# Performance work log

Measured on AMD Instinct MI355X. Metric: run time of the kernel, lower is better.

The kernel has to match this reference:

```python
import jax, jax.numpy as jnp
import numpy as np

EPS = 1e-6
NUM_SPECIAL = 4
NUM_HEADS = 16


def _rms_norm(x, w, eps=EPS):
    # x: [..., d], normalize over last dim
    var = jnp.mean(jnp.square(x), axis=-1, keepdims=True)
    return x * jax.lax.rsqrt(var + eps) * w


def _rotate_half(x):
    d = x.shape[-1] // 2
    return jnp.concatenate([-x[..., d:], x[..., :d]], axis=-1)


def _apply_rotary(q, k, cos, sin):
    # q,k: [B,H,N,hd]; cos,sin: [N,hd] -> broadcast [1,1,N,hd]
    cos = cos[None, None, :, :]
    sin = sin[None, None, :, :]
    q_out = q * cos + _rotate_half(q) * sin
    k_out = k * cos + _rotate_half(k) * sin
    return q_out, k_out


def _make_2d_mask(seq_len, num_special, window):
    # special tokens attend / are attended fully; patches use 2D local box
    patch_len = seq_len - num_special
    gs = int(round(patch_len ** 0.5))
    idx = jnp.arange(seq_len)
    special = idx < num_special
    p = idx - num_special
    row = p // gs
    col = p % gs
    special_case = special[:, None] | special[None, :]
    swa = (jnp.abs(row[:, None] - row[None, :]) <= window) & (
        jnp.abs(col[:, None] - col[None, :]) <= window)
    return special_case | swa  # [N, N] bool


def setup_inputs() -> dict:
    key = jax.random.key(0)
    ks = jax.random.split(key, 7)
    B, N, C = 4, 1028, 1024
    hd = C // NUM_HEADS
    return {
        "hidden_states": jax.random.normal(ks[0], (B, N, C), dtype=jnp.float32),
        "cos": jax.random.uniform(ks[1], (N, hd), dtype=jnp.float32),
        "sin": jax.random.uniform(ks[2], (N, hd), dtype=jnp.float32),
        "qkv_w": jax.random.normal(ks[3], (3 * C, C), dtype=jnp.float32) * (C ** -0.5),
        "out_w": jax.random.normal(ks[4], (C, C), dtype=jnp.float32) * (C ** -0.5),
        "norm_q_w": jnp.ones((hd,), dtype=jnp.float32),
        "norm_k_w": jnp.ones((hd,), dtype=jnp.float32),
        "sliding_window": 2,
    }


def reference(hidden_states, cos, sin, qkv_w, out_w, norm_q_w, norm_k_w, sliding_window):
    B, N, C = hidden_states.shape
    H = NUM_HEADS
    hd = C // H

    # fused QKV projection (nn.Linear: x @ W^T)
    qkv = jnp.einsum('bnc,dc->bnd', hidden_states, qkv_w)
    qkv = qkv.reshape(B, N, 3, H, hd).transpose(2, 0, 3, 1, 4)  # [3,B,H,N,hd]
    q, k, v = qkv[0], qkv[1], qkv[2]

    # per-head-dim RMSNorm on q and k
    q = _rms_norm(q, norm_q_w)
    k = _rms_norm(k, norm_k_w)

    # RoPE
    q, k = _apply_rotary(q, k, cos, sin)

    # 2D sliding-window + special-token mask
    mask = _make_2d_mask(N, NUM_SPECIAL, sliding_window)  # [N,N]

    scale = 1.0 / jnp.sqrt(jnp.asarray(hd, dtype=q.dtype))
    scores = jnp.einsum('bhqd,bhkd->bhqk', q, k) * scale
    neg = jnp.asarray(jnp.finfo(scores.dtype).min, dtype=scores.dtype)
    scores = jnp.where(mask[None, None, :, :], scores, neg)
    probs = jax.nn.softmax(scores, axis=-1)
    attn = jnp.einsum('bhqk,bhkd->bhqd', probs, v)  # [B,H,N,hd]

    attn = attn.transpose(0, 2, 1, 3).reshape(B, N, C)
    return jnp.einsum('bnc,dc->bnd', attn, out_w)
```

## Files before the change

kernel.cpp:

```cpp
#include <hip/hip_runtime.h>
#include <hip/hip_bf16.h>
#include <stdint.h>

typedef __bf16 bf16;
typedef __attribute__((ext_vector_type(8))) __bf16 bf16x8;
typedef __attribute__((ext_vector_type(4))) __bf16 bf16x4;
typedef __attribute__((ext_vector_type(4))) float f32x4;

#define NSEQ 1028
#define CDIM 1024
#define NHEADS 16
#define HD 64
#define BHN 64
#define NPAD 1088
#define M_REAL 4112
#define M_PAD 4224

static __device__ __forceinline__ void async_copy16(bf16* lds, const bf16* g) {
  __builtin_amdgcn_global_load_lds(
      (const __attribute__((address_space(1))) uint32_t*)g,
      (__attribute__((address_space(3))) uint32_t*)lds, 16, 0, 0);
}

__global__ __launch_bounds__(256) void cast_pad_kernel(const float* __restrict__ src,
                                                       bf16* __restrict__ dst,
                                                       long n_src, long n_dst) {
  long t = (long)blockIdx.x * 256 + threadIdx.x;
  long stride = (long)gridDim.x * 256;
  for (long j = t * 4; j < n_dst; j += stride * 4) {
    bf16x4 o;
    if (j + 4 <= n_src) {
      float4 v = *(const float4*)(src + j);
      o[0] = (bf16)v.x; o[1] = (bf16)v.y; o[2] = (bf16)v.z; o[3] = (bf16)v.w;
    } else {
      for (int k = 0; k < 4; k++) o[k] = (bf16)((j + k < n_src) ? src[j + k] : 0.0f);
    }
    *(bf16x4*)(dst + j) = o;
  }
}

template <int EPI>
__global__ __launch_bounds__(256) void gemm_bf16_kernel(
    const bf16* __restrict__ A, const bf16* __restrict__ Bm, int K, int N, int Mreal,
    bf16* __restrict__ q_bf, bf16* __restrict__ k_bf, bf16* __restrict__ v_raw,
    float* __restrict__ outF,
    const float* __restrict__ cosb, const float* __restrict__ sinb,
    const float* __restrict__ nqw, const float* __restrict__ nkw) {
  __shared__ __attribute__((aligned(16))) bf16 As[2][128 * 64];
  __shared__ __attribute__((aligned(16))) bf16 Bs[2][128 * 64];
  const int tid = threadIdx.x;
  const int lane = tid & 63;
  const int wid = tid >> 6;
  const int wr = wid >> 1, wc = wid & 1;
  const int l15 = lane & 15, l4 = lane >> 4;

  const int nwg = gridDim.x;
  const int cpx = nwg >> 3;
  const int work = (blockIdx.x & 7) * cpx + (blockIdx.x >> 3);
  const int ntx = N >> 7;
  const int n0 = (work % ntx) << 7;
  const int m0 = (work / ntx) << 7;

  f32x4 acc[4][4] = {};

  size_t a_base[4], b_base[4];
#pragma unroll
  for (int s = 0; s < 4; s++) {
    int c = tid + s * 256;
    int row = c >> 3, ch = c & 7;
    int chs = ch ^ (row & 7);
    a_base[s] = (size_t)(m0 + row) * K + (chs << 3);
    b_base[s] = (size_t)(n0 + row) * K + (chs << 3);
  }

#define STAGE(bufi, ktof)                                         \
  {                                                               \
    _Pragma("unroll")                                             \
    for (int s = 0; s < 4; s++) {                                 \
      int c = tid + s * 256;                                      \
      async_copy16(&As[bufi][c * 8], A + a_base[s] + (ktof));     \
      async_copy16(&Bs[bufi][c * 8], Bm + b_base[s] + (ktof));    \
    }                                                             \
  }

  const int nt = K >> 6;
  STAGE(0, 0);

  for (int t = 0; t < nt; ++t) {
    if (t + 1 < nt) {
      STAGE((t + 1) & 1, (t + 1) << 6);
      asm volatile("s_waitcnt vmcnt(8)" ::: "memory");
    } else {
      asm volatile("s_waitcnt vmcnt(0)" ::: "memory");
    }
    __builtin_amdgcn_s_barrier();

    const int rsw = l15 & 7;
    const int cur = t & 1;
    bf16x8 af[2][4], bfr[2][4];
#pragma unroll
    for (int h = 0; h < 2; h++)
#pragma unroll
      for (int i = 0; i < 4; i++)
        af[h][i] = *(const bf16x8*)&As[cur][(wr * 64 + i * 16 + l15) * 64 +
                                            (((h * 4 + l4) ^ rsw) << 3)];
#pragma unroll
    for (int h = 0; h < 2; h++)
#pragma unroll
      for (int j = 0; j < 4; j++)
        bfr[h][j] = *(const bf16x8*)&Bs[cur][(wc * 64 + j * 16 + l15) * 64 +
                                             (((h * 4 + l4) ^ rsw) << 3)];

#pragma unroll
    for (int h = 0; h < 2; h++)
#pragma unroll
      for (int i = 0; i < 4; i++)
#pragma unroll
        for (int j = 0; j < 4; j++)
          acc[i][j] = __builtin_amdgcn_mfma_f32_16x16x32_bf16(af[h][i], bfr[h][j], acc[i][j], 0, 0, 0);

    asm volatile("s_waitcnt lgkmcnt(0)" ::: "memory");
    __builtin_amdgcn_s_barrier();
  }
#undef STAGE

  if (EPI == 0) {
    const int d_base = n0 + wc * 64;
    const int t = d_base >> 10;
    const int hh = (d_base & 1023) >> 6;
    if (t == 2) {
#pragma unroll
      for (int i = 0; i < 4; i++)
#pragma unroll
        for (int r = 0; r < 4; r++) {
          int m = m0 + wr * 64 + i * 16 + l4 * 4 + r;
          if (m < Mreal) {
            int b = m / NSEQ, n = m % NSEQ;
            size_t rb = ((size_t)(b * NHEADS + hh) * NSEQ + n) * HD;
#pragma unroll
            for (int j = 0; j < 4; j++)
              v_raw[rb + j * 16 + l15] = (bf16)acc[i][j][r];
          }
        }
    } else {
      const float* wn = (t == 0) ? nqw : nkw;
      bf16* dst = (t == 0) ? q_bf : k_bf;
      float wv[4];
#pragma unroll
      for (int j = 0; j < 4; j++) wv[j] = wn[j * 16 + l15];
#pragma unroll
      for (int i = 0; i < 4; i++)
#pragma unroll
        for (int r = 0; r < 4; r++) {
          int m = m0 + wr * 64 + i * 16 + l4 * 4 + r;
          if (m >= Mreal) continue;
          float ss = 0.0f;
#pragma unroll
          for (int j = 0; j < 4; j++) { float x = acc[i][j][r]; ss += x * x; }
          ss += __shfl_xor(ss, 1);
          ss += __shfl_xor(ss, 2);
          ss += __shfl_xor(ss, 4);
          ss += __shfl_xor(ss, 8);
          float rms = rsqrtf(ss * (1.0f / HD) + 1e-6f);
          int b = m / NSEQ, n = m % NSEQ;
          float qn[4];
#pragma unroll
          for (int j = 0; j < 4; j++) qn[j] = acc[i][j][r] * rms * wv[j];
          size_t rb = ((size_t)(b * NHEADS + hh) * NPAD + n) * HD;
#pragma unroll
          for (int j = 0; j < 4; j++) {
            float c = cosb[n * HD + j * 16 + l15];
            float s = sinb[n * HD + j * 16 + l15];
            float rot = (j < 2) ? -qn[j + 2] : qn[j - 2];
            dst[rb + j * 16 + l15] = (bf16)(qn[j] * c + rot * s);
          }
        }
    }
  } else {
#pragma unroll
    for (int i = 0; i < 4; i++)
#pragma unroll
      for (int j = 0; j < 4; j++) {
        int d = n0 + wc * 64 + j * 16 + l15;
        int mrow = m0 + wr * 64 + i * 16 + l4 * 4;
#pragma unroll
        for (int r = 0; r < 4; r++) {
          int m = mrow + r;
          if (m < Mreal) outF[(size_t)m * N + d] = acc[i][j][r];
        }
      }
  }
}

__global__ __launch_bounds__(256) void v_transpose_kernel(const bf16* __restrict__ v_raw,
                                                          bf16* __restrict__ vT) {
  __shared__ bf16 tile[64][65];
  int bh = blockIdx.y, c = blockIdx.x;
  int tid = threadIdx.x;
#pragma unroll
  for (int jj = 0; jj < 16; jj++) {
    int idx = tid + jj * 256;
    int i = idx >> 6, e = idx & 63;
    int n = (c == 0) ? i : (64 * c - 60 + i);
    bool ok = (c == 0) ? (i < 4) : (n < NSEQ);
    tile[i][e] = ok ? v_raw[((size_t)bh * NSEQ + n) * HD + e] : (bf16)0.0f;
  }
  __syncthreads();
#pragma unroll
  for (int jj = 0; jj < 16; jj++) {
    int idx = tid + jj * 256;
    int e = idx >> 6, i = idx & 63;
    vT[((size_t)bh * HD + e) * NPAD + 64 * c + i] = tile[i][e];
  }
}

__global__ __launch_bounds__(256) void attn_kernel(
    const bf16* __restrict__ Q, const bf16* __restrict__ Kb, const bf16* __restrict__ Vt,
    bf16* __restrict__ att, const int* __restrict__ winp) {
  __shared__ __attribute__((aligned(16))) bf16 P_s[4][16][72];
  __shared__ float o_s[4][4][64];
  __shared__ float ml_s[4][2][16];
  const int bh = blockIdx.y, qt = blockIdx.x;
  const int W = winp[0];
  const int tid = threadIdx.x, w = tid >> 6, lane = tid & 63;
  const int l15 = lane & 15, l4 = lane >> 4;
  const size_t qkbase = (size_t)bh * NPAD * HD;
  const size_t vtb = (size_t)bh * HD * NPAD;
  const bool is_spec = (qt == 16);

  const int qrow0 = is_spec ? 0 : (4 + qt * 64 + w * 16);
  bf16x8 aq0 = *(const bf16x8*)&Q[qkbase + (size_t)(qrow0 + l15) * HD + l4 * 8];
  bf16x8 aq1 = *(const bf16x8*)&Q[qkbase + (size_t)(qrow0 + l15) * HD + 32 + l4 * 8];

  float mrow[4], lrow[4];
  f32x4 o[4] = {};
#pragma unroll
  for (int r = 0; r < 4; r++) { mrow[r] = -1e30f; lrow[r] = 0.0f; }

  int p0, pstep, pmax, toff;
  if (is_spec) {
    p0 = w; pstep = 4; pmax = 16; toff = -1;
  } else {
    int ta = ((2 * qt - W + 64) >> 1) - 32;
    int tb = (2 * qt + 1 + W) >> 1;
    ta = ta < 0 ? 0 : ta;
    tb = tb > 15 ? 15 : tb;
    p0 = 0; pstep = 1; pmax = tb - ta + 1; toff = ta - 1;
  }

  for (int p = p0; p <= pmax; p += pstep) {
    const bool sp = (p == 0);
    const int tau = toff + p;
    const int krow0 = sp ? 0 : (4 + tau * 64);
    const int vcol0 = sp ? 0 : (64 + tau * 64);

    f32x4 sacc[4] = {};
#pragma unroll
    for (int kf = 0; kf < 4; kf++) {
      const bf16* kp = &Kb[qkbase + (size_t)(krow0 + kf * 16 + l15) * HD];
      bf16x8 b0 = *(const bf16x8*)(kp + l4 * 8);
      bf16x8 b1 = *(const bf16x8*)(kp + 32 + l4 * 8);
      sacc[kf] = __builtin_amdgcn_mfma_f32_16x16x32_bf16(aq0, b0, sacc[kf], 0, 0, 0);
      sacc[kf] = __builtin_amdgcn_mfma_f32_16x16x32_bf16(aq1, b1, sacc[kf], 0, 0, 0);
    }

    float pvv[4][4];
#pragma unroll
    for (int kf = 0; kf < 4; kf++)
#pragma unroll
      for (int r = 0; r < 4; r++) {
        float s = sacc[kf][r] * 0.125f;
        bool valid;
        if (sp) {
          valid = (kf == 0) && (l15 < 4);
        } else if (is_spec) {
          valid = true;
        } else {
          int p_k = tau * 64 + kf * 16 + l15;
          int p_q = qt * 64 + w * 16 + l4 * 4 + r;
          int dr = (p_q >> 5) - (p_k >> 5); dr = dr < 0 ? -dr : dr;
          int dc = (p_q & 31) - (p_k & 31); dc = dc < 0 ? -dc : dc;
          valid = (dr <= W) && (dc <= W);
        }
        pvv[kf][r] = valid ? s : -1e30f;
      }

#pragma unroll
    for (int r = 0; r < 4; r++) {
      float mx = fmaxf(fmaxf(pvv[0][r], pvv[1][r]), fmaxf(pvv[2][r], pvv[3][r]));
#pragma unroll
      for (int mm = 1; mm < 16; mm <<= 1) mx = fmaxf(mx, __shfl_xor(mx, mm));
      float mnew = fmaxf(mrow[r], mx);
      float scale = __expf(mrow[r] - mnew);
      float rs = 0.0f;
#pragma unroll
      for (int kf = 0; kf < 4; kf++) {
        float pp = __expf(pvv[kf][r] - mnew);
        pvv[kf][r] = pp;
        rs += pp;
      }
#pragma unroll
      for (int mm = 1; mm < 16; mm <<= 1) rs += __shfl_xor(rs, mm);
      lrow[r] = lrow[r] * scale + rs;
      mrow[r] = mnew;
#pragma unroll
      for (int f = 0; f < 4; f++) o[f][r] *= scale;
    }

#pragma unroll
    for (int kf = 0; kf < 4; kf++)
#pragma unroll
      for (int r = 0; r < 4; r++)
        P_s[w][l4 * 4 + r][kf * 16 + l15] = (bf16)pvv[kf][r];

    bf16x8 pa0 = *(const bf16x8*)&P_s[w][l15][l4 * 8];
    bf16x8 pa1 = *(const bf16x8*)&P_s[w][l15][32 + l4 * 8];
#pragma unroll
    for (int f = 0; f < 4; f++) {
      const bf16* vp = &Vt[vtb + (size_t)(f * 16 + l15) * NPAD + vcol0];
      bf16x8 v0 = *(const bf16x8*)(vp + l4 * 8);
      bf16x8 v1 = *(const bf16x8*)(vp + 32 + l4 * 8);
      o[f] = __builtin_amdgcn_mfma_f32_16x16x32_bf16(pa0, v0, o[f], 0, 0, 0);
      o[f] = __builtin_amdgcn_mfma_f32_16x16x32_bf16(pa1, v1, o[f], 0, 0, 0);
    }
  }

  const int b = bh >> 4, h = bh & 15;
  if (!is_spec) {
#pragma unroll
    for (int f = 0; f < 4; f++)
#pragma unroll
      for (int r = 0; r < 4; r++) {
        int n = qrow0 + l4 * 4 + r;
        att[((size_t)(b * NSEQ + n)) * CDIM + h * HD + f * 16 + l15] =
            (bf16)(o[f][r] / lrow[r]);
      }
  } else {
    if (l4 == 0) {
#pragma unroll
      for (int f = 0; f < 4; f++)
#pragma unroll
        for (int r = 0; r < 4; r++) o_s[w][r][f * 16 + l15] = o[f][r];
      if (l15 == 0)
#pragma unroll
        for (int r = 0; r < 4; r++) { ml_s[w][0][r] = mrow[r]; ml_s[w][1][r] = lrow[r]; }
    }
    __syncthreads();
    int row = tid >> 6, dim = tid & 63;
    float M = -1e30f;
#pragma unroll
    for (int ww = 0; ww < 4; ww++) M = fmaxf(M, ml_s[ww][0][row]);
    float L = 0.0f, val = 0.0f;
#pragma unroll
    for (int ww = 0; ww < 4; ww++) {
      float e = __expf(ml_s[ww][0][row] - M);
      L += e * ml_s[ww][1][row];
      val += e * o_s[ww][row][dim];
    }
    att[((size_t)(b * NSEQ + row)) * CDIM + h * HD + dim] = (bf16)(val / L);
  }
}

extern "C" void kernel_launch(void* const* d_in, const int* in_sizes, int n_in,
                              void* d_out, int out_size, void* d_ws, size_t ws_size,
                              hipStream_t stream) {
  const float* hidden = (const float*)d_in[0];
  const float* cosb = (const float*)d_in[1];
  const float* sinb = (const float*)d_in[2];
  const float* qkv_w = (const float*)d_in[3];
  const float* out_w = (const float*)d_in[4];
  const float* norm_q_w = (const float*)d_in[5];
  const float* norm_k_w = (const float*)d_in[6];
  const int* win = (const int*)d_in[7];
  float* out = (float*)d_out;

  char* ws = (char*)d_ws;
  size_t off = 0;
  auto alloc = [&](size_t bytes) {
    char* p = ws + off;
    off += (bytes + 255) & ~(size_t)255;
    return p;
  };
  bf16* A_bf  = (bf16*)alloc((size_t)M_PAD * CDIM * 2);
  bf16* W1    = (bf16*)alloc((size_t)3 * CDIM * CDIM * 2);
  bf16* W2    = (bf16*)alloc((size_t)CDIM * CDIM * 2);
  bf16* v_raw = (bf16*)alloc((size_t)BHN * NSEQ * HD * 2);
  bf16* q_bf  = (bf16*)alloc((size_t)BHN * NPAD * HD * 2);
  bf16* k_bf  = (bf16*)alloc((size_t)BHN * NPAD * HD * 2);
  bf16* vT    = (bf16*)alloc((size_t)BHN * HD * NPAD * 2);
  bf16* att   = (bf16*)alloc((size_t)M_PAD * CDIM * 2);
  (void)ws_size; (void)in_sizes; (void)n_in; (void)out_size;

  cast_pad_kernel<<<2048, 256, 0, stream>>>(hidden, A_bf, (long)M_REAL * CDIM, (long)M_PAD * CDIM);
  cast_pad_kernel<<<1024, 256, 0, stream>>>(qkv_w, W1, (long)3 * CDIM * CDIM, (long)3 * CDIM * CDIM);
  cast_pad_kernel<<<512, 256, 0, stream>>>(out_w, W2, (long)CDIM * CDIM, (long)CDIM * CDIM);

  gemm_bf16_kernel<0><<<792, 256, 0, stream>>>(
      A_bf, W1, CDIM, 3 * CDIM, M_REAL, q_bf, k_bf, v_raw, nullptr,
      cosb, sinb, norm_q_w, norm_k_w);
  v_transpose_kernel<<<dim3(17, 64), 256, 0, stream>>>(v_raw, vT);
  attn_kernel<<<dim3(17, 64), 256, 0, stream>>>(q_bf, k_bf, vT, att, win);
  gemm_bf16_kernel<1><<<264, 256, 0, stream>>>(
      att, W2, CDIM, CDIM, M_REAL, nullptr, nullptr, nullptr, out,
      nullptr, nullptr, nullptr, nullptr);
}
```

Before: 136.7 us.

## Use 256x256-tile 8-wave GEMM with interleaved staging for QKV projection

Replaces the 128x128 QKV GEMM with a dedicated 256x256-tile kernel using 512 threads and 8 waves. It interleaves LDS fragment loads, async global-to-LDS staging and MFMA quadrants, with setprio and barriers between them. The aim is higher data reuse per tile and better overlap of memory and compute. The A buffer is padded to a multiple of 256 rows, and the grid drops to 204 blocks, which may leave some of the 256 CUs idle. The output GEMM becomes a separate non-templated kernel with unchanged behaviour.

```diff
diff --git a/kernel.cpp b/kernel.cpp
--- a/kernel.cpp
+++ b/kernel.cpp
@@ -15,6 +15,7 @@
 #define NPAD 1088
 #define M_REAL 4112
 #define M_PAD 4224
+#define M_PAD256 4352
 
 static __device__ __forceinline__ void async_copy16(bf16* lds, const bf16* g) {
   __builtin_amdgcn_global_load_lds(
@@ -39,13 +40,177 @@
   }
 }
 
-template <int EPI>
-__global__ __launch_bounds__(256) void gemm_bf16_kernel(
-    const bf16* __restrict__ A, const bf16* __restrict__ Bm, int K, int N, int Mreal,
+__global__ __launch_bounds__(512, 2) void gemm_qkv_256(
+    const bf16* __restrict__ A, const bf16* __restrict__ Bm,
     bf16* __restrict__ q_bf, bf16* __restrict__ k_bf, bf16* __restrict__ v_raw,
-    float* __restrict__ outF,
     const float* __restrict__ cosb, const float* __restrict__ sinb,
     const float* __restrict__ nqw, const float* __restrict__ nkw) {
+  constexpr int K = CDIM;
+  constexpr int NT = K / 64;
+  __shared__ __attribute__((aligned(16))) bf16 As[2 * 2 * 128 * 64];
+  __shared__ __attribute__((aligned(16))) bf16 Bs[2 * 2 * 128 * 64];
+  const int tid = threadIdx.x;
+  const int lane = tid & 63;
+  const int wid = tid >> 6;
+  const int wr = wid >> 2;
+  const int wc = wid & 3;
+  const int l15 = lane & 15, l4 = lane >> 4;
+  const int rsw = l15 & 7;
+
+  const int nwg = gridDim.x;
+  const int qq = nwg >> 3, rr = nwg & 7;
+  const int xcd = blockIdx.x & 7, pos = blockIdx.x >> 3;
+  const int work = (xcd < rr ? xcd * (qq + 1) : rr * (qq + 1) + (xcd - rr) * qq) + pos;
+  const int n0 = (work % 12) << 8;
+  const int m0 = (work / 12) << 8;
+
+  f32x4 acc[8][4] = {};
+  bf16x8 afr[4][2], bfr0[2][2], bfr1[2][2];
+
+  size_t a_src[2], b_src[2];
+#pragma unroll
+  for (int s = 0; s < 2; s++) {
+    int idx = tid + s * 512;
+    int row = idx >> 3, ch = idx & 7, chs = ch ^ (row & 7);
+    a_src[s] = (size_t)(m0 + row) * K + (chs << 3);
+    b_src[s] = (size_t)(n0 + row) * K + (chs << 3);
+  }
+
+#define STAGE_A(bufi, h, tt)                                                   \
+  { _Pragma("unroll") for (int s = 0; s < 2; s++)                              \
+      async_copy16(&As[((bufi) * 2 + (h)) * 8192 + (tid + s * 512) * 8],       \
+                   A + a_src[s] + (size_t)(h) * (128 * K) + (size_t)(tt) * 64); }
+#define STAGE_B(bufi, h, tt)                                                   \
+  { _Pragma("unroll") for (int s = 0; s < 2; s++)                              \
+      async_copy16(&Bs[((bufi) * 2 + (h)) * 8192 + (tid + s * 512) * 8],       \
+                   Bm + b_src[s] + (size_t)(h) * (128 * K) + (size_t)(tt) * 64); }
+#define LDA_FRAG(mq)                                                           \
+  { _Pragma("unroll") for (int ii = 0; ii < 4; ii++)                           \
+      _Pragma("unroll") for (int kk = 0; kk < 2; kk++)                         \
+        afr[ii][kk] = *(const bf16x8*)&As[abase + (((mq)*4 + ii) * 16 + l15) * 64 + \
+                                          (((kk * 4 + l4) ^ rsw) << 3)]; }
+#define LDB_FRAG(dst, nq)                                                      \
+  { _Pragma("unroll") for (int jj = 0; jj < 2; jj++)                           \
+      _Pragma("unroll") for (int kk = 0; kk < 2; kk++)                         \
+        dst[jj][kk] = *(const bf16x8*)&Bs[bbase + ((wc & 1) * 64 + ((nq)*2 + jj) * 16 + l15) * 64 + \
+                                          (((kk * 4 + l4) ^ rsw) << 3)]; }
+#define MFMA_Q(mq, nq, bb)                                                     \
+  { _Pragma("unroll") for (int ii = 0; ii < 4; ii++)                           \
+      _Pragma("unroll") for (int jj = 0; jj < 2; jj++)                         \
+        _Pragma("unroll") for (int kk = 0; kk < 2; kk++)                       \
+          acc[(mq)*4 + ii][(nq)*2 + jj] = __builtin_amdgcn_mfma_f32_16x16x32_bf16( \
+              afr[ii][kk], bb[jj][kk], acc[(mq)*4 + ii][(nq)*2 + jj], 0, 0, 0); }
+
+  STAGE_A(0, 0, 0); STAGE_A(0, 1, 0); STAGE_B(0, 0, 0); STAGE_B(0, 1, 0);
+  STAGE_B(1, 0, 1); STAGE_B(1, 1, 1);
+  asm volatile("s_waitcnt vmcnt(4)" ::: "memory");
+  __builtin_amdgcn_s_barrier();
+
+  for (int t = 0; t < NT; ++t) {
+    const int cur = t & 1, nxt = cur ^ 1;
+    const int abase = (cur * 2 + wr) * 8192;
+    const int bbase = (cur * 2 + (wc >> 1)) * 8192;
+    LDA_FRAG(0); LDB_FRAG(bfr0, 0);
+    if (t + 1 < NT) STAGE_A(nxt, 0, t + 1);
+    __builtin_amdgcn_s_barrier();
+    asm volatile("s_waitcnt lgkmcnt(0)" ::: "memory");
+    __builtin_amdgcn_sched_barrier(0);
+    __builtin_amdgcn_s_setprio(1);
+    MFMA_Q(0, 0, bfr0);
+    __builtin_amdgcn_s_setprio(0);
+    __builtin_amdgcn_s_barrier();
+    LDB_FRAG(bfr1, 1);
+    if (t + 1 < NT) STAGE_A(nxt, 1, t + 1);
+    __builtin_amdgcn_s_barrier();
+    asm volatile("s_waitcnt lgkmcnt(0)" ::: "memory");
+    __builtin_amdgcn_sched_barrier(0);
+    __builtin_amdgcn_s_setprio(1);
+    MFMA_Q(0, 1, bfr1);
+    __builtin_amdgcn_s_setprio(0);
+    __builtin_amdgcn_s_barrier();
+    LDA_FRAG(1);
+    if (t + 2 < NT) STAGE_B(cur, 0, t + 2);
+    __builtin_amdgcn_s_barrier();
+    asm volatile("s_waitcnt lgkmcnt(0)" ::: "memory");
+    __builtin_amdgcn_sched_barrier(0);
+    __builtin_amdgcn_s_setprio(1);
+    MFMA_Q(1, 0, bfr0);
+    __builtin_amdgcn_s_setprio(0);
+    __builtin_amdgcn_s_barrier();
+    if (t + 2 < NT) {
+      STAGE_B(cur, 1, t + 2);
+      asm volatile("s_waitcnt vmcnt(4)" ::: "memory");
+    } else {
+      asm volatile("s_waitcnt vmcnt(0)" ::: "memory");
+    }
+    __builtin_amdgcn_s_barrier();
+    __builtin_amdgcn_s_setprio(1);
+    MFMA_Q(1, 1, bfr1);
+    __builtin_amdgcn_s_setprio(0);
+    __builtin_amdgcn_s_barrier();
+  }
+#undef STAGE_A
+#undef STAGE_B
+#undef LDA_FRAG
+#undef LDB_FRAG
+#undef MFMA_Q
+
+  const int d_base = n0 + wc * 64;
+  const int tsel = d_base >> 10;
+  const int hh = (d_base & 1023) >> 6;
+  if (tsel == 2) {
+#pragma unroll
+    for (int i = 0; i < 8; i++)
+#pragma unroll
+      for (int r = 0; r < 4; r++) {
+        int m = m0 + wr * 128 + i * 16 + l4 * 4 + r;
+        if (m < M_REAL) {
+          int b = m / NSEQ, n = m % NSEQ;
+          size_t rb = ((size_t)(b * NHEADS + hh) * NSEQ + n) * HD;
+#pragma unroll
+          for (int j = 0; j < 4; j++)
+            v_raw[rb + j * 16 + l15] = (bf16)acc[i][j][r];
+        }
+      }
+  } else {
+    const float* wn = (tsel == 0) ? nqw : nkw;
+    bf16* dst = (tsel == 0) ? q_bf : k_bf;
+    float wv[4];
+#pragma unroll
+    for (int j = 0; j < 4; j++) wv[j] = wn[j * 16 + l15];
+#pragma unroll
+    for (int i = 0; i < 8; i++)
+#pragma unroll
+      for (int r = 0; r < 4; r++) {
+        int m = m0 + wr * 128 + i * 16 + l4 * 4 + r;
+        if (m >= M_REAL) continue;
+        float ss = 0.0f;
+#pragma unroll
+        for (int j = 0; j < 4; j++) { float x = acc[i][j][r]; ss += x * x; }
+        ss += __shfl_xor(ss, 1);
+        ss += __shfl_xor(ss, 2);
+        ss += __shfl_xor(ss, 4);
+        ss += __shfl_xor(ss, 8);
+        float rms = rsqrtf(ss * (1.0f / HD) + 1e-6f);
+        int b = m / NSEQ, n = m % NSEQ;
+        float qn[4];
+#pragma unroll
+        for (int j = 0; j < 4; j++) qn[j] = acc[i][j][r] * rms * wv[j];
+        size_t rb = ((size_t)(b * NHEADS + hh) * NPAD + n) * HD;
+#pragma unroll
+        for (int j = 0; j < 4; j++) {
+          float c = cosb[n * HD + j * 16 + l15];
+          float s = sinb[n * HD + j * 16 + l15];
+          float rot = (j < 2) ? -qn[j + 2] : qn[j - 2];
+          dst[rb + j * 16 + l15] = (bf16)(qn[j] * c + rot * s);
+        }
+      }
+  }
+}
+
+__global__ __launch_bounds__(256) void gemm_out_kernel(
+    const bf16* __restrict__ A, const bf16* __restrict__ Bm, int K, int N, int Mreal,
+    float* __restrict__ outF) {
   __shared__ __attribute__((aligned(16))) bf16 As[2][128 * 64];
   __shared__ __attribute__((aligned(16))) bf16 Bs[2][128 * 64];
   const int tid = threadIdx.x;
@@ -124,72 +289,18 @@
   }
 #undef STAGE
 
-  if (EPI == 0) {
-    const int d_base = n0 + wc * 64;
-    const int t = d_base >> 10;
-    const int hh = (d_base & 1023) >> 6;
-    if (t == 2) {
-#pragma unroll
-      for (int i = 0; i < 4; i++)
-#pragma unroll
-        for (int r = 0; r < 4; r++) {
-          int m = m0 + wr * 64 + i * 16 + l4 * 4 + r;
-          if (m < Mreal) {
-            int b = m / NSEQ, n = m % NSEQ;
-            size_t rb = ((size_t)(b * NHEADS + hh) * NSEQ + n) * HD;
-#pragma unroll
-            for (int j = 0; j < 4; j++)
-              v_raw[rb + j * 16 + l15] = (bf16)acc[i][j][r];
-          }
-        }
-    } else {
-      const float* wn = (t == 0) ? nqw : nkw;
-      bf16* dst = (t == 0) ? q_bf : k_bf;
-      float wv[4];
-#pragma unroll
-      for (int j = 0; j < 4; j++) wv[j] = wn[j * 16 + l15];
-#pragma unroll
-      for (int i = 0; i < 4; i++)
-#pragma unroll
-        for (int r = 0; r < 4; r++) {
-          int m = m0 + wr * 64 + i * 16 + l4 * 4 + r;
-          if (m >= Mreal) continue;
-          float ss = 0.0f;
-#pragma unroll
-          for (int j = 0; j < 4; j++) { float x = acc[i][j][r]; ss += x * x; }
-          ss += __shfl_xor(ss, 1);
-          ss += __shfl_xor(ss, 2);
-          ss += __shfl_xor(ss, 4);
-          ss += __shfl_xor(ss, 8);
-          float rms = rsqrtf(ss * (1.0f / HD) + 1e-6f);
-          int b = m / NSEQ, n = m % NSEQ;
-          float qn[4];
-#pragma unroll
-          for (int j = 0; j < 4; j++) qn[j] = acc[i][j][r] * rms * wv[j];
-          size_t rb = ((size_t)(b * NHEADS + hh) * NPAD + n) * HD;
-#pragma unroll
-          for (int j = 0; j < 4; j++) {
-            float c = cosb[n * HD + j * 16 + l15];
-            float s = sinb[n * HD + j * 16 + l15];
-            float rot = (j < 2) ? -qn[j + 2] : qn[j - 2];
-            dst[rb + j * 16 + l15] = (bf16)(qn[j] * c + rot * s);
-          }
-        }
-    }
-  } else {
-#pragma unroll
-    for (int i = 0; i < 4; i++)
-#pragma unroll
-      for (int j = 0; j < 4; j++) {
-        int d = n0 + wc * 64 + j * 16 + l15;
-        int mrow = m0 + wr * 64 + i * 16 + l4 * 4;
-#pragma unroll
-        for (int r = 0; r < 4; r++) {
-          int m = mrow + r;
-          if (m < Mreal) outF[(size_t)m * N + d] = acc[i][j][r];
-        }
+#pragma unroll
+  for (int i = 0; i < 4; i++)
+#pragma unroll
+    for (int j = 0; j < 4; j++) {
+      int d = n0 + wc * 64 + j * 16 + l15;
+      int mrow = m0 + wr * 64 + i * 16 + l4 * 4;
+#pragma unroll
+      for (int r = 0; r < 4; r++) {
+        int m = mrow + r;
+        if (m < Mreal) outF[(size_t)m * N + d] = acc[i][j][r];
       }
-  }
+    }
 }
 
 __global__ __launch_bounds__(256) void v_transpose_kernel(const bf16* __restrict__ v_raw,
@@ -381,7 +492,7 @@
     off += (bytes + 255) & ~(size_t)255;
     return p;
   };
-  bf16* A_bf  = (bf16*)alloc((size_t)M_PAD * CDIM * 2);
+  bf16* A_bf  = (bf16*)alloc((size_t)M_PAD256 * CDIM * 2);
   bf16* W1    = (bf16*)alloc((size_t)3 * CDIM * CDIM * 2);
   bf16* W2    = (bf16*)alloc((size_t)CDIM * CDIM * 2);
   bf16* v_raw = (bf16*)alloc((size_t)BHN * NSEQ * HD * 2);
@@ -391,16 +502,13 @@
   bf16* att   = (bf16*)alloc((size_t)M_PAD * CDIM * 2);
   (void)ws_size; (void)in_sizes; (void)n_in; (void)out_size;
 
-  cast_pad_kernel<<<2048, 256, 0, stream>>>(hidden, A_bf, (long)M_REAL * CDIM, (long)M_PAD * CDIM);
+  cast_pad_kernel<<<2048, 256, 0, stream>>>(hidden, A_bf, (long)M_REAL * CDIM, (long)M_PAD256 * CDIM);
   cast_pad_kernel<<<1024, 256, 0, stream>>>(qkv_w, W1, (long)3 * CDIM * CDIM, (long)3 * CDIM * CDIM);
   cast_pad_kernel<<<512, 256, 0, stream>>>(out_w, W2, (long)CDIM * CDIM, (long)CDIM * CDIM);
 
-  gemm_bf16_kernel<0><<<792, 256, 0, stream>>>(
-      A_bf, W1, CDIM, 3 * CDIM, M_REAL, q_bf, k_bf, v_raw, nullptr,
-      cosb, sinb, norm_q_w, norm_k_w);
+  gemm_qkv_256<<<204, 512, 0, stream>>>(A_bf, W1, q_bf, k_bf, v_raw,
+                                        cosb, sinb, norm_q_w, norm_k_w);
   v_transpose_kernel<<<dim3(17, 64), 256, 0, stream>>>(v_raw, vT);
   attn_kernel<<<dim3(17, 64), 256, 0, stream>>>(q_bf, k_bf, vT, att, win);
-  gemm_bf16_kernel<1><<<264, 256, 0, stream>>>(
-      att, W2, CDIM, CDIM, M_REAL, nullptr, nullptr, nullptr, out,
-      nullptr, nullptr, nullptr, nullptr);
-}
+  gemm_out_kernel<<<264, 256, 0, stream>>>(att, W2, CDIM, CDIM, M_REAL, out);
+}
```

New measurement: 135.3 us. No clear change (-1.0%).
